# Optimization experiments

Measured on AMD Instinct MI355X. Metric: run time of the kernel, lower is better.

## Reference

```python
import jax, jax.numpy as jnp
import numpy as np

EPS = 1e-8

def _cosine_sim_to_codebook(x, codebook):
    # x: [N, D], codebook: [K, D] -> [N, K]; equivalent to broadcast F.cosine_similarity
    xn = x / jnp.maximum(jnp.linalg.norm(x, axis=-1, keepdims=True), EPS)
    cn = codebook / jnp.maximum(jnp.linalg.norm(codebook, axis=-1, keepdims=True), EPS)
    return xn @ cn.T

def _gumbel_softmax(key, logits, tau, hard):
    g = jax.random.gumbel(key, logits.shape, dtype=logits.dtype)
    y = jax.nn.softmax((logits + g) / tau, axis=-1)
    if hard:
        onehot = jax.nn.one_hot(jnp.argmax(y, axis=-1), logits.shape[-1], dtype=y.dtype)
        # straight-through estimator
        y = onehot + y - jax.lax.stop_gradient(y)
    return y

def setup_inputs() -> dict:
    key = jax.random.key(0)
    k1, k2, k3 = jax.random.split(key, 3)
    B, L, D, K = 64, 512, 512, 1024
    N = B * L
    return {
        "state_emb": jax.random.normal(k1, (N, D), dtype=jnp.float32),
        "adv_emb": jax.random.normal(k2, (N, D), dtype=jnp.float32),
        "codebook": jax.random.normal(k3, (K, D), dtype=jnp.float32),
        "B": B,
        "L": L,
    }

def reference(state_emb, adv_emb, codebook, B, L):
    tau = 1.0
    alpha = 0.5
    # NOTE: the original computes adv_emb_shift but never uses it (dead code); omitted.
    sim_state = _cosine_sim_to_codebook(state_emb, codebook)  # [N, K]
    sim_adv = _cosine_sim_to_codebook(adv_emb, codebook)      # [N, K]
    sim = alpha * sim_state + (1.0 - alpha) * sim_adv
    gk = jax.random.key(42)
    gk1, gk2 = jax.random.split(gk)
    weights_hard = _gumbel_softmax(gk1, sim, tau, hard=True)   # [N, K] one-hot (ST)
    weights_soft = _gumbel_softmax(gk2, sim, tau, hard=False)  # [N, K]
    indices = jnp.argmax(weights_hard, axis=-1)[:, None]       # [N, 1]
    z_q = weights_hard @ codebook                              # [N, D]
    return (z_q, weights_soft, indices)
```

## Files before the change

kernel.cpp:

```cpp
#include <hip/hip_runtime.h>
#include <stdint.h>

typedef unsigned int u32;
typedef unsigned short u16;
typedef __attribute__((ext_vector_type(8))) __bf16 bf16x8;
typedef __attribute__((ext_vector_type(4))) float f32x4;

#define N_ROWS 32768
#define D_DIM 512
#define K_CB 1024

__host__ __device__ inline void tf2x32(u32 k0, u32 k1, u32 x0, u32 x1, u32 &o0, u32 &o1) {
  const u32 ks2 = k0 ^ k1 ^ 0x1BD11BDAu;
#define TFR(r) x0 += x1; x1 = (x1 << (r)) | (x1 >> (32 - (r))); x1 ^= x0;
  x0 += k0; x1 += k1;
  TFR(13) TFR(15) TFR(26) TFR(6)
  x0 += k1; x1 += ks2 + 1u;
  TFR(17) TFR(29) TFR(16) TFR(24)
  x0 += ks2; x1 += k0 + 2u;
  TFR(13) TFR(15) TFR(26) TFR(6)
  x0 += k0; x1 += k1 + 3u;
  TFR(17) TFR(29) TFR(16) TFR(24)
  x0 += k1; x1 += ks2 + 4u;
  TFR(13) TFR(15) TFR(26) TFR(6)
  x0 += ks2; x1 += k0 + 5u;
#undef TFR
  o0 = x0; o1 = x1;
}

__device__ inline float gumbel_fast(u32 bits) {
  const float f = __uint_as_float((bits >> 9) | 0x3f800000u) - 1.0f;
  const float tiny = 1.17549435e-38f;
  const float u = fmaxf(tiny, f + tiny);
  const float NLN2 = -0.69314718055994530942f;
  const float a = __log2f(u);
  const float v = a * NLN2;
  const float b = __log2f(v);
  return b * NLN2;
}

__device__ inline u16 f32_bf16(float x) {
  u32 u = __float_as_uint(x);
  u += 0x7fffu + ((u >> 16) & 1u);
  return (u16)(u >> 16);
}
__device__ inline float bf16_f32(u16 h) { return __uint_as_float(((u32)h) << 16); }

__global__ void __launch_bounds__(256) prep_codebook(const float* __restrict__ cb,
                                                     u16* __restrict__ cn_hi,
                                                     u16* __restrict__ cn_lo) {
  const int lane = threadIdx.x & 63, wid = threadIdx.x >> 6;
  const int row = blockIdx.x * 4 + wid;
  const float* src = cb + (size_t)row * D_DIM;
  float v[8]; float ss = 0.f;
#pragma unroll
  for (int i = 0; i < 8; ++i) { v[i] = src[lane + 64 * i]; ss = fmaf(v[i], v[i], ss); }
#pragma unroll
  for (int off = 32; off; off >>= 1) ss += __shfl_xor(ss, off);
  const float denom = fmaxf(sqrtf(ss), 1e-8f);
#pragma unroll
  for (int i = 0; i < 8; ++i) {
    const float x = v[i] / denom;
    const u16 h = f32_bf16(x);
    const u16 l = f32_bf16(x - bf16_f32(h));
    cn_hi[(size_t)row * D_DIM + lane + 64 * i] = h;
    cn_lo[(size_t)row * D_DIM + lane + 64 * i] = l;
  }
}

__global__ void __launch_bounds__(256) prep_m(const float* __restrict__ se,
                                              const float* __restrict__ ae,
                                              u16* __restrict__ m_hi,
                                              u16* __restrict__ m_lo) {
  const int lane = threadIdx.x & 63, wid = threadIdx.x >> 6;
  const size_t row = (size_t)blockIdx.x * 4 + wid;
  const float* s = se + row * D_DIM;
  const float* a = ae + row * D_DIM;
  float sv[8], av[8]; float ss = 0.f, sa = 0.f;
#pragma unroll
  for (int i = 0; i < 8; ++i) {
    sv[i] = s[lane + 64 * i]; av[i] = a[lane + 64 * i];
    ss = fmaf(sv[i], sv[i], ss); sa = fmaf(av[i], av[i], sa);
  }
#pragma unroll
  for (int off = 32; off; off >>= 1) { ss += __shfl_xor(ss, off); sa += __shfl_xor(sa, off); }
  const float ds = fmaxf(sqrtf(ss), 1e-8f);
  const float da = fmaxf(sqrtf(sa), 1e-8f);
#pragma unroll
  for (int i = 0; i < 8; ++i) {
    const float m = 0.5f * (sv[i] / ds) + 0.5f * (av[i] / da);
    const u16 h = f32_bf16(m);
    const u16 l = f32_bf16(m - bf16_f32(h));
    m_hi[row * D_DIM + lane + 64 * i] = h;
    m_lo[row * D_DIM + lane + 64 * i] = l;
  }
}

__global__ void __launch_bounds__(256) gemm_sim(const u16* __restrict__ mA_hi,
                                                const u16* __restrict__ mA_lo,
                                                const u16* __restrict__ cn_hi,
                                                const u16* __restrict__ cn_lo,
                                                float* __restrict__ sim) {
  __shared__ __align__(16) u16 As_hi[128 * 64];
  __shared__ __align__(16) u16 As_lo[128 * 64];
  __shared__ __align__(16) u16 Bs_hi[128 * 64];
  __shared__ __align__(16) u16 Bs_lo[128 * 64];

  const int tid = threadIdx.x;
  const int lane = tid & 63;
  const int wid = tid >> 6;
  const int wr = wid >> 1, wc = wid & 1;
  const int bn = blockIdx.x, bm = blockIdx.y;

  const int fr = lane & 15;
  const int q8 = lane >> 4;

  f32x4 acc[4][4];
#pragma unroll
  for (int i = 0; i < 4; ++i)
#pragma unroll
    for (int j = 0; j < 4; ++j) acc[i][j] = (f32x4){0.f, 0.f, 0.f, 0.f};

  const int o_base = wid * 1024 + lane * 16;
  const char* gA_hi = (const char*)mA_hi + (size_t)(bm * 128) * (D_DIM * 2);
  const char* gA_lo = (const char*)mA_lo + (size_t)(bm * 128) * (D_DIM * 2);
  const char* gB_hi = (const char*)cn_hi + (size_t)(bn * 128) * (D_DIM * 2);
  const char* gB_lo = (const char*)cn_lo + (size_t)(bn * 128) * (D_DIM * 2);

  for (int kt = 0; kt < D_DIM / 64; ++kt) {
    const int kbyte = kt * 128;
#pragma unroll
    for (int i = 0; i < 4; ++i) {
      const int o = o_base + i * 4096;
      const int row = o >> 7;
      const int cbyt = o & 127;
      const size_t goff = (size_t)row * (D_DIM * 2) + kbyte + cbyt;
      const int loff = wid * 1024 + i * 4096;
      __builtin_amdgcn_global_load_lds((const __attribute__((address_space(1))) void*)(gA_hi + goff),
                                       (__attribute__((address_space(3))) void*)((char*)As_hi + loff), 16, 0, 0);
      __builtin_amdgcn_global_load_lds((const __attribute__((address_space(1))) void*)(gA_lo + goff),
                                       (__attribute__((address_space(3))) void*)((char*)As_lo + loff), 16, 0, 0);
      __builtin_amdgcn_global_load_lds((const __attribute__((address_space(1))) void*)(gB_hi + goff),
                                       (__attribute__((address_space(3))) void*)((char*)Bs_hi + loff), 16, 0, 0);
      __builtin_amdgcn_global_load_lds((const __attribute__((address_space(1))) void*)(gB_lo + goff),
                                       (__attribute__((address_space(3))) void*)((char*)Bs_lo + loff), 16, 0, 0);
    }
    __syncthreads();

#pragma unroll
    for (int kk = 0; kk < 2; ++kk) {
      bf16x8 ah[4], al[4], bh[4], bl[4];
      const int co = kk * 32 + q8 * 8;
#pragma unroll
      for (int mi = 0; mi < 4; ++mi) {
        const int r = wr * 64 + mi * 16 + fr;
        ah[mi] = *(const bf16x8*)&As_hi[r * 64 + co];
        al[mi] = *(const bf16x8*)&As_lo[r * 64 + co];
      }
#pragma unroll
      for (int ni = 0; ni < 4; ++ni) {
        const int r = wc * 64 + ni * 16 + fr;
        bh[ni] = *(const bf16x8*)&Bs_hi[r * 64 + co];
        bl[ni] = *(const bf16x8*)&Bs_lo[r * 64 + co];
      }
#pragma unroll
      for (int mi = 0; mi < 4; ++mi)
#pragma unroll
        for (int ni = 0; ni < 4; ++ni) {
          acc[mi][ni] = __builtin_amdgcn_mfma_f32_16x16x32_bf16(ah[mi], bh[ni], acc[mi][ni], 0, 0, 0);
          acc[mi][ni] = __builtin_amdgcn_mfma_f32_16x16x32_bf16(ah[mi], bl[ni], acc[mi][ni], 0, 0, 0);
          acc[mi][ni] = __builtin_amdgcn_mfma_f32_16x16x32_bf16(al[mi], bh[ni], acc[mi][ni], 0, 0, 0);
        }
    }
    __syncthreads();
  }

  const int row_base = bm * 128 + wr * 64 + q8 * 4;
  const int col_base = bn * 128 + wc * 64 + fr;
#pragma unroll
  for (int mi = 0; mi < 4; ++mi)
#pragma unroll
    for (int ni = 0; ni < 4; ++ni) {
      const int r0 = row_base + mi * 16;
      const int c = col_base + ni * 16;
#pragma unroll
      for (int r = 0; r < 4; ++r)
        sim[(size_t)(r0 + r) * K_CB + c] = acc[mi][ni][r];
    }
}

__global__ void __launch_bounds__(256) gumbel_epilogue(float* __restrict__ simw,
                                                       float* __restrict__ zq,
                                                       float* __restrict__ idxf,
                                                       const float* __restrict__ cb,
                                                       u32 k1a, u32 k1b, u32 k2a, u32 k2b) {
  const int lane = threadIdx.x & 63, wid = threadIdx.x >> 6;
  const int n = blockIdx.x * 4 + wid;
  float4* row4 = (float4*)(simw + (size_t)n * K_CB);
  const u32 kbase = (u32)n * K_CB;

  float p2[16];
  float ps = 0.f;
  float bv = -1e30f; int bi = 0;
#pragma unroll
  for (int i = 0; i < 4; ++i) {
    const int f4i = lane + i * 64;
    const float4 s4 = row4[f4i];
#pragma unroll
    for (int j = 0; j < 4; ++j) {
      const u32 k = 4u * (u32)f4i + (u32)j;
      u32 a0, a1, b0, b1;
      tf2x32(k1a, k1b, 0u, kbase + k, a0, a1);
      tf2x32(k2a, k2b, 0u, kbase + k, b0, b1);
      const float s = (j == 0) ? s4.x : (j == 1) ? s4.y : (j == 2) ? s4.z : s4.w;
      const float l1 = s + gumbel_fast(a0 ^ a1);
      const float l2 = s + gumbel_fast(b0 ^ b1);
      const float p = __expf(l2);
      p2[i * 4 + j] = p;
      ps += p;
      if (l1 > bv) { bv = l1; bi = (int)k; }
    }
  }
#pragma unroll
  for (int off = 1; off < 64; off <<= 1) {
    const float ov = __shfl_xor(bv, off);
    const int oi = __shfl_xor(bi, off);
    if (ov > bv || (ov == bv && oi < bi)) { bv = ov; bi = oi; }
    ps += __shfl_xor(ps, off);
  }
  const float inv = 1.0f / ps;
#pragma unroll
  for (int i = 0; i < 4; ++i) {
    float4 o;
    o.x = p2[i * 4 + 0] * inv;
    o.y = p2[i * 4 + 1] * inv;
    o.z = p2[i * 4 + 2] * inv;
    o.w = p2[i * 4 + 3] * inv;
    row4[lane + i * 64] = o;
  }
  const float4* crow = (const float4*)(cb + (size_t)bi * D_DIM);
  float4* zrow = (float4*)(zq + (size_t)n * D_DIM);
#pragma unroll
  for (int i = 0; i < 2; ++i) zrow[lane + i * 64] = crow[lane + i * 64];
  if (lane == 0) idxf[n] = (float)bi;
}

extern "C" void kernel_launch(void* const* d_in, const int* in_sizes, int n_in,
                              void* d_out, int out_size, void* d_ws, size_t ws_size,
                              hipStream_t stream) {
  const float* state = (const float*)d_in[0];
  const float* adv = (const float*)d_in[1];
  const float* cb = (const float*)d_in[2];

  char* ws = (char*)d_ws;
  u16* m_hi = (u16*)ws;
  u16* m_lo = (u16*)(ws + (size_t)N_ROWS * D_DIM * 2);
  u16* cn_hi = (u16*)(ws + (size_t)N_ROWS * D_DIM * 4);
  u16* cn_lo = (u16*)(ws + (size_t)N_ROWS * D_DIM * 4 + (size_t)K_CB * D_DIM * 2);

  float* zq = (float*)d_out;
  float* simw = zq + (size_t)N_ROWS * D_DIM;
  float* idxf = simw + (size_t)N_ROWS * K_CB;

  u32 gk1a, gk1b, gk2a, gk2b;
  tf2x32(0u, 42u, 0u, 0u, gk1a, gk1b);
  tf2x32(0u, 42u, 0u, 1u, gk2a, gk2b);

  hipLaunchKernelGGL(prep_codebook, dim3(K_CB / 4), dim3(256), 0, stream, cb, cn_hi, cn_lo);
  hipLaunchKernelGGL(prep_m, dim3(N_ROWS / 4), dim3(256), 0, stream, state, adv, m_hi, m_lo);
  hipLaunchKernelGGL(gemm_sim, dim3(K_CB / 128, N_ROWS / 128), dim3(256), 0, stream,
                     m_hi, m_lo, cn_hi, cn_lo, simw);
  hipLaunchKernelGGL(gumbel_epilogue, dim3(N_ROWS / 4), dim3(256), 0, stream,
                     simw, zq, idxf, cb, gk1a, gk1b, gk2a, gk2b);
}
```

Before: 528.0 us.

## Fuse Gumbel sampling into GEMM epilogue with atomic row reductions

Moves the Threefry RNG, Gumbel noise, exp and per-row argmax/sum from a separate pass into the GEMM epilogue. Partial row sums and packed argmax keys are combined across column tiles with atomicAdd and a 64-bit atomicMax. A lighter normalize-and-gather kernel then rescales the row and copies the chosen codebook row. The aim is to avoid writing and rereading the full similarity matrix and to overlap RNG ALU work with the GEMM, at the cost of atomics, two memsets and the normalize pass still rereading the weights. The prep kernels are also vectorized and the rotate uses alignbit.

```diff
diff --git a/kernel.cpp b/kernel.cpp
--- a/kernel.cpp
+++ b/kernel.cpp
@@ -3,6 +3,7 @@
 
 typedef unsigned int u32;
 typedef unsigned short u16;
+typedef unsigned long long u64;
 typedef __attribute__((ext_vector_type(8))) __bf16 bf16x8;
 typedef __attribute__((ext_vector_type(4))) float f32x4;
 
@@ -10,9 +11,17 @@
 #define D_DIM 512
 #define K_CB 1024
 
+__host__ __device__ inline u32 rotl32(u32 x, int r) {
+#ifdef __HIP_DEVICE_COMPILE__
+  return __builtin_amdgcn_alignbit(x, x, 32 - r);
+#else
+  return (x << r) | (x >> (32 - r));
+#endif
+}
+
 __host__ __device__ inline void tf2x32(u32 k0, u32 k1, u32 x0, u32 x1, u32 &o0, u32 &o1) {
   const u32 ks2 = k0 ^ k1 ^ 0x1BD11BDAu;
-#define TFR(r) x0 += x1; x1 = (x1 << (r)) | (x1 >> (32 - (r))); x1 ^= x0;
+#define TFR(r) x0 += x1; x1 = rotl32(x1, r); x1 ^= x0;
   x0 += k0; x1 += k1;
   TFR(13) TFR(15) TFR(26) TFR(6)
   x0 += k1; x1 += ks2 + 1u;
@@ -35,8 +44,7 @@
   const float NLN2 = -0.69314718055994530942f;
   const float a = __log2f(u);
   const float v = a * NLN2;
-  const float b = __log2f(v);
-  return b * NLN2;
+  return __log2f(v) * NLN2;
 }
 
 __device__ inline u16 f32_bf16(float x) {
@@ -51,20 +59,30 @@
                                                      u16* __restrict__ cn_lo) {
   const int lane = threadIdx.x & 63, wid = threadIdx.x >> 6;
   const int row = blockIdx.x * 4 + wid;
-  const float* src = cb + (size_t)row * D_DIM;
-  float v[8]; float ss = 0.f;
-#pragma unroll
-  for (int i = 0; i < 8; ++i) { v[i] = src[lane + 64 * i]; ss = fmaf(v[i], v[i], ss); }
+  const float4* src = (const float4*)(cb + (size_t)row * D_DIM);
+  float4 v[2]; float ss = 0.f;
+#pragma unroll
+  for (int i = 0; i < 2; ++i) {
+    v[i] = src[lane + 64 * i];
+    ss = fmaf(v[i].x, v[i].x, ss); ss = fmaf(v[i].y, v[i].y, ss);
+    ss = fmaf(v[i].z, v[i].z, ss); ss = fmaf(v[i].w, v[i].w, ss);
+  }
 #pragma unroll
   for (int off = 32; off; off >>= 1) ss += __shfl_xor(ss, off);
-  const float denom = fmaxf(sqrtf(ss), 1e-8f);
-#pragma unroll
-  for (int i = 0; i < 8; ++i) {
-    const float x = v[i] / denom;
-    const u16 h = f32_bf16(x);
-    const u16 l = f32_bf16(x - bf16_f32(h));
-    cn_hi[(size_t)row * D_DIM + lane + 64 * i] = h;
-    cn_lo[(size_t)row * D_DIM + lane + 64 * i] = l;
+  const float inv = 1.0f / fmaxf(sqrtf(ss), 1e-8f);
+  ushort4* dhi = (ushort4*)(cn_hi + (size_t)row * D_DIM);
+  ushort4* dlo = (ushort4*)(cn_lo + (size_t)row * D_DIM);
+#pragma unroll
+  for (int i = 0; i < 2; ++i) {
+    const float c[4] = {v[i].x * inv, v[i].y * inv, v[i].z * inv, v[i].w * inv};
+    ushort4 h4, l4;
+    u16* hp = (u16*)&h4; u16* lp = (u16*)&l4;
+#pragma unroll
+    for (int j = 0; j < 4; ++j) {
+      const u16 h = f32_bf16(c[j]);
+      hp[j] = h; lp[j] = f32_bf16(c[j] - bf16_f32(h));
+    }
+    dhi[lane + 64 * i] = h4; dlo[lane + 64 * i] = l4;
   }
 }
 
@@ -74,33 +92,46 @@
                                               u16* __restrict__ m_lo) {
   const int lane = threadIdx.x & 63, wid = threadIdx.x >> 6;
   const size_t row = (size_t)blockIdx.x * 4 + wid;
-  const float* s = se + row * D_DIM;
-  const float* a = ae + row * D_DIM;
-  float sv[8], av[8]; float ss = 0.f, sa = 0.f;
-#pragma unroll
-  for (int i = 0; i < 8; ++i) {
+  const float4* s = (const float4*)(se + row * D_DIM);
+  const float4* a = (const float4*)(ae + row * D_DIM);
+  float4 sv[2], av[2]; float ss = 0.f, sa = 0.f;
+#pragma unroll
+  for (int i = 0; i < 2; ++i) {
     sv[i] = s[lane + 64 * i]; av[i] = a[lane + 64 * i];
-    ss = fmaf(sv[i], sv[i], ss); sa = fmaf(av[i], av[i], sa);
+    ss = fmaf(sv[i].x, sv[i].x, ss); ss = fmaf(sv[i].y, sv[i].y, ss);
+    ss = fmaf(sv[i].z, sv[i].z, ss); ss = fmaf(sv[i].w, sv[i].w, ss);
+    sa = fmaf(av[i].x, av[i].x, sa); sa = fmaf(av[i].y, av[i].y, sa);
+    sa = fmaf(av[i].z, av[i].z, sa); sa = fmaf(av[i].w, av[i].w, sa);
   }
 #pragma unroll
   for (int off = 32; off; off >>= 1) { ss += __shfl_xor(ss, off); sa += __shfl_xor(sa, off); }
-  const float ds = fmaxf(sqrtf(ss), 1e-8f);
-  const float da = fmaxf(sqrtf(sa), 1e-8f);
-#pragma unroll
-  for (int i = 0; i < 8; ++i) {
-    const float m = 0.5f * (sv[i] / ds) + 0.5f * (av[i] / da);
-    const u16 h = f32_bf16(m);
-    const u16 l = f32_bf16(m - bf16_f32(h));
-    m_hi[row * D_DIM + lane + 64 * i] = h;
-    m_lo[row * D_DIM + lane + 64 * i] = l;
-  }
-}
-
-__global__ void __launch_bounds__(256) gemm_sim(const u16* __restrict__ mA_hi,
-                                                const u16* __restrict__ mA_lo,
-                                                const u16* __restrict__ cn_hi,
-                                                const u16* __restrict__ cn_lo,
-                                                float* __restrict__ sim) {
+  const float is = 0.5f / fmaxf(sqrtf(ss), 1e-8f);
+  const float ia = 0.5f / fmaxf(sqrtf(sa), 1e-8f);
+  ushort4* dhi = (ushort4*)(m_hi + row * D_DIM);
+  ushort4* dlo = (ushort4*)(m_lo + row * D_DIM);
+#pragma unroll
+  for (int i = 0; i < 2; ++i) {
+    const float c[4] = {sv[i].x * is + av[i].x * ia, sv[i].y * is + av[i].y * ia,
+                        sv[i].z * is + av[i].z * ia, sv[i].w * is + av[i].w * ia};
+    ushort4 h4, l4;
+    u16* hp = (u16*)&h4; u16* lp = (u16*)&l4;
+#pragma unroll
+    for (int j = 0; j < 4; ++j) {
+      const u16 h = f32_bf16(c[j]);
+      hp[j] = h; lp[j] = f32_bf16(c[j] - bf16_f32(h));
+    }
+    dhi[lane + 64 * i] = h4; dlo[lane + 64 * i] = l4;
+  }
+}
+
+__global__ void __launch_bounds__(256) fused_gemm_gumbel(const u16* __restrict__ mA_hi,
+                                                         const u16* __restrict__ mA_lo,
+                                                         const u16* __restrict__ cn_hi,
+                                                         const u16* __restrict__ cn_lo,
+                                                         float* __restrict__ pw,
+                                                         float* __restrict__ ps_arr,
+                                                         u64* __restrict__ bvpk,
+                                                         u32 k1a, u32 k1b, u32 k2a, u32 k2b) {
   __shared__ __align__(16) u16 As_hi[128 * 64];
   __shared__ __align__(16) u16 As_lo[128 * 64];
   __shared__ __align__(16) u16 Bs_hi[128 * 64];
@@ -175,68 +206,62 @@
     __syncthreads();
   }
 
-  const int row_base = bm * 128 + wr * 64 + q8 * 4;
-  const int col_base = bn * 128 + wc * 64 + fr;
-#pragma unroll
-  for (int mi = 0; mi < 4; ++mi)
-#pragma unroll
-    for (int ni = 0; ni < 4; ++ni) {
-      const int r0 = row_base + mi * 16;
-      const int c = col_base + ni * 16;
-#pragma unroll
-      for (int r = 0; r < 4; ++r)
-        sim[(size_t)(r0 + r) * K_CB + c] = acc[mi][ni][r];
-    }
-}
-
-__global__ void __launch_bounds__(256) gumbel_epilogue(float* __restrict__ simw,
-                                                       float* __restrict__ zq,
-                                                       float* __restrict__ idxf,
-                                                       const float* __restrict__ cb,
-                                                       u32 k1a, u32 k1b, u32 k2a, u32 k2b) {
+  const u32 nrow0 = (u32)bm * 128u;
+  const u32 col0 = (u32)(bn * 128 + wc * 64 + fr);
+#pragma unroll
+  for (int mi = 0; mi < 4; ++mi) {
+#pragma unroll
+    for (int r = 0; r < 4; ++r) {
+      const u32 n = nrow0 + (u32)(wr * 64 + mi * 16 + q8 * 4 + r);
+      const u32 kb = n * (u32)K_CB;
+      float psum = 0.f; float lbv = -1e30f; u32 lbi = 0u;
+#pragma unroll
+      for (int ni = 0; ni < 4; ++ni) {
+        const u32 k = col0 + (u32)(ni * 16);
+        const float s = acc[mi][ni][r];
+        u32 a0, a1, b0, b1;
+        tf2x32(k1a, k1b, 0u, kb + k, a0, a1);
+        tf2x32(k2a, k2b, 0u, kb + k, b0, b1);
+        const float l1 = s + gumbel_fast(a0 ^ a1);
+        const float p = __expf(s + gumbel_fast(b0 ^ b1));
+        pw[(size_t)kb + k] = p;
+        psum += p;
+        if (l1 > lbv) { lbv = l1; lbi = k; }
+      }
+#pragma unroll
+      for (int off = 1; off < 16; off <<= 1) {
+        const float ov = __shfl_xor(lbv, off);
+        const u32 oi = (u32)__shfl_xor((int)lbi, off);
+        psum += __shfl_xor(psum, off);
+        if (ov > lbv || (ov == lbv && oi < lbi)) { lbv = ov; lbi = oi; }
+      }
+      if (fr == 0) {
+        atomicAdd(&ps_arr[n], psum);
+        const u32 sb = __float_as_uint(lbv);
+        const u32 key = (sb & 0x80000000u) ? ~sb : (sb | 0x80000000u);
+        const u64 pk = ((u64)key << 32) | (u64)(~lbi);
+        atomicMax(&bvpk[n], pk);
+      }
+    }
+  }
+}
+
+__global__ void __launch_bounds__(256) norm_gather(float* __restrict__ w,
+                                                   float* __restrict__ zq,
+                                                   float* __restrict__ idxf,
+                                                   const float* __restrict__ ps_arr,
+                                                   const u64* __restrict__ bvpk,
+                                                   const float* __restrict__ cb) {
   const int lane = threadIdx.x & 63, wid = threadIdx.x >> 6;
   const int n = blockIdx.x * 4 + wid;
-  float4* row4 = (float4*)(simw + (size_t)n * K_CB);
-  const u32 kbase = (u32)n * K_CB;
-
-  float p2[16];
-  float ps = 0.f;
-  float bv = -1e30f; int bi = 0;
+  const float inv = 1.0f / ps_arr[n];
+  const u32 bi = ~((u32)bvpk[n]);
+  float4* row4 = (float4*)(w + (size_t)n * K_CB);
 #pragma unroll
   for (int i = 0; i < 4; ++i) {
-    const int f4i = lane + i * 64;
-    const float4 s4 = row4[f4i];
-#pragma unroll
-    for (int j = 0; j < 4; ++j) {
-      const u32 k = 4u * (u32)f4i + (u32)j;
-      u32 a0, a1, b0, b1;
-      tf2x32(k1a, k1b, 0u, kbase + k, a0, a1);
-      tf2x32(k2a, k2b, 0u, kbase + k, b0, b1);
-      const float s = (j == 0) ? s4.x : (j == 1) ? s4.y : (j == 2) ? s4.z : s4.w;
-      const float l1 = s + gumbel_fast(a0 ^ a1);
-      const float l2 = s + gumbel_fast(b0 ^ b1);
-      const float p = __expf(l2);
-      p2[i * 4 + j] = p;
-      ps += p;
-      if (l1 > bv) { bv = l1; bi = (int)k; }
-    }
-  }
-#pragma unroll
-  for (int off = 1; off < 64; off <<= 1) {
-    const float ov = __shfl_xor(bv, off);
-    const int oi = __shfl_xor(bi, off);
-    if (ov > bv || (ov == bv && oi < bi)) { bv = ov; bi = oi; }
-    ps += __shfl_xor(ps, off);
-  }
-  const float inv = 1.0f / ps;
-#pragma unroll
-  for (int i = 0; i < 4; ++i) {
-    float4 o;
-    o.x = p2[i * 4 + 0] * inv;
-    o.y = p2[i * 4 + 1] * inv;
-    o.z = p2[i * 4 + 2] * inv;
-    o.w = p2[i * 4 + 3] * inv;
-    row4[lane + i * 64] = o;
+    float4 v = row4[lane + i * 64];
+    v.x *= inv; v.y *= inv; v.z *= inv; v.w *= inv;
+    row4[lane + i * 64] = v;
   }
   const float4* crow = (const float4*)(cb + (size_t)bi * D_DIM);
   float4* zrow = (float4*)(zq + (size_t)n * D_DIM);
@@ -253,23 +278,28 @@
   const float* cb = (const float*)d_in[2];
 
   char* ws = (char*)d_ws;
-  u16* m_hi = (u16*)ws;
-  u16* m_lo = (u16*)(ws + (size_t)N_ROWS * D_DIM * 2);
-  u16* cn_hi = (u16*)(ws + (size_t)N_ROWS * D_DIM * 4);
-  u16* cn_lo = (u16*)(ws + (size_t)N_ROWS * D_DIM * 4 + (size_t)K_CB * D_DIM * 2);
+  size_t off = 0;
+  u16* m_hi = (u16*)(ws + off); off += (size_t)N_ROWS * D_DIM * 2;
+  u16* m_lo = (u16*)(ws + off); off += (size_t)N_ROWS * D_DIM * 2;
+  u16* cn_hi = (u16*)(ws + off); off += (size_t)K_CB * D_DIM * 2;
+  u16* cn_lo = (u16*)(ws + off); off += (size_t)K_CB * D_DIM * 2;
+  float* ps_arr = (float*)(ws + off); off += (size_t)N_ROWS * 4;
+  u64* bvpk = (u64*)(ws + off); off += (size_t)N_ROWS * 8;
 
   float* zq = (float*)d_out;
-  float* simw = zq + (size_t)N_ROWS * D_DIM;
-  float* idxf = simw + (size_t)N_ROWS * K_CB;
+  float* w = zq + (size_t)N_ROWS * D_DIM;
+  float* idxf = w + (size_t)N_ROWS * K_CB;
 
   u32 gk1a, gk1b, gk2a, gk2b;
   tf2x32(0u, 42u, 0u, 0u, gk1a, gk1b);
   tf2x32(0u, 42u, 0u, 1u, gk2a, gk2b);
 
+  hipMemsetAsync(ps_arr, 0, (size_t)N_ROWS * 4, stream);
+  hipMemsetAsync(bvpk, 0, (size_t)N_ROWS * 8, stream);
   hipLaunchKernelGGL(prep_codebook, dim3(K_CB / 4), dim3(256), 0, stream, cb, cn_hi, cn_lo);
   hipLaunchKernelGGL(prep_m, dim3(N_ROWS / 4), dim3(256), 0, stream, state, adv, m_hi, m_lo);
-  hipLaunchKernelGGL(gemm_sim, dim3(K_CB / 128, N_ROWS / 128), dim3(256), 0, stream,
-                     m_hi, m_lo, cn_hi, cn_lo, simw);
-  hipLaunchKernelGGL(gumbel_epilogue, dim3(N_ROWS / 4), dim3(256), 0, stream,
-                     simw, zq, idxf, cb, gk1a, gk1b, gk2a, gk2b);
-}
+  hipLaunchKernelGGL(fused_gemm_gumbel, dim3(K_CB / 128, N_ROWS / 128), dim3(256), 0, stream,
+                     m_hi, m_lo, cn_hi, cn_lo, w, ps_arr, bvpk, gk1a, gk1b, gk2a, gk2b);
+  hipLaunchKernelGGL(norm_gather, dim3(N_ROWS / 4), dim3(256), 0, stream,
+                     w, zq, idxf, ps_arr, bvpk, cb);
+}
```

Result: slower. 678.1 us (+28.4%).
